# Kernel optimization log

Measured on AMD Instinct MI355X. Metric: run time of the kernel, lower is better.

Reference implementation:

```python
import jax, jax.numpy as jnp
import numpy as np


def setup_inputs() -> dict:
    key = jax.random.key(0)
    k_x, k_f1, k_f2, k_b = jax.random.split(key, 4)
    N, D = 2097152, 64  # batch rows, in_features = out_features = 8*8
    x = jax.random.normal(k_x, (N, D), dtype=jnp.float32)
    factor1 = jax.random.normal(k_f1, (8, 8), dtype=jnp.float32)
    factor2 = jax.random.normal(k_f2, (8, 8), dtype=jnp.float32)
    bias = jax.random.normal(k_b, (D,), dtype=jnp.float32)
    return {"x": x, "factor1": factor1, "factor2": factor2, "bias": bias}


def reference(x, factor1, factor2, bias):
    # weight = kron(ones((1,1)), factor1, factor2) == kron(factor1, factor2)
    # shape: [8*8, 8*8] = [64, 64]
    w = jnp.kron(factor1, factor2)
    # F.linear(x, w, bias) = x @ w.T + bias
    return x @ w.T + bias
```

## Files before the change

### kernel.cpp

```cpp
#include <hip/hip_runtime.h>


__global__ __launch_bounds__(256) void kron_linear_kernel(
    const float* __restrict__ x,
    const float* __restrict__ f1,
    const float* __restrict__ f2,
    const float* __restrict__ bias,
    float* __restrict__ out,
    int n_rows)
{
    int row = blockIdx.x * 256 + threadIdx.x;
    if (row >= n_rows) return;

    const float* xr = x + (size_t)row * 64;
    float* orow = out + (size_t)row * 64;

    float T[8][8];
#pragma unroll
    for (int i1 = 0; i1 < 8; ++i1) {
        float4 a = *(const float4*)(xr + i1 * 8);
        float4 b = *(const float4*)(xr + i1 * 8 + 4);
        float xv[8] = {a.x, a.y, a.z, a.w, b.x, b.y, b.z, b.w};
#pragma unroll
        for (int j2 = 0; j2 < 8; ++j2) {
            float acc = 0.f;
#pragma unroll
            for (int i2 = 0; i2 < 8; ++i2)
                acc += xv[i2] * f2[j2 * 8 + i2];
            T[i1][j2] = acc;
        }
    }

#pragma unroll
    for (int j1 = 0; j1 < 8; ++j1) {
        float o[8];
#pragma unroll
        for (int j2 = 0; j2 < 8; ++j2) o[j2] = bias[j1 * 8 + j2];
#pragma unroll
        for (int i1 = 0; i1 < 8; ++i1) {
            float w = f1[j1 * 8 + i1];
#pragma unroll
            for (int j2 = 0; j2 < 8; ++j2)
                o[j2] += w * T[i1][j2];
        }
        float4 s0 = {o[0], o[1], o[2], o[3]};
        float4 s1 = {o[4], o[5], o[6], o[7]};
        *(float4*)(orow + j1 * 8)     = s0;
        *(float4*)(orow + j1 * 8 + 4) = s1;
    }
}

extern "C" void kernel_launch(void* const* d_in, const int* in_sizes, int n_in,
                              void* d_out, int out_size, void* d_ws, size_t ws_size,
                              hipStream_t stream) {
    const float* x    = (const float*)d_in[0];
    const float* f1   = (const float*)d_in[1];
    const float* f2   = (const float*)d_in[2];
    const float* bias = (const float*)d_in[3];
    float* out = (float*)d_out;

    int n_rows = out_size / 64;
    int blocks = (n_rows + 255) / 256;
    kron_linear_kernel<<<blocks, 256, 0, stream>>>(x, f1, f2, bias, out, n_rows);
}
```

Baseline: 996.5 us.

## Stage row tiles through swizzled LDS for coalesced loads and stores

Each block now handles 128 rows. It copies the input tile into LDS with direct global-to-LDS 16-byte loads using an XOR swizzle, so global reads are fully coalesced. The computation is split across two threads per row, each producing half of the output columns. Results are written back to LDS and then stored to global memory coalesced. This adds barriers and 32KB of LDS per block, which may limit occupancy, and keeps a fallback path for the partial tail tile.

```diff
diff --git a/kernel.cpp b/kernel.cpp
--- a/kernel.cpp
+++ b/kernel.cpp
@@ -1,7 +1,12 @@
 #include <hip/hip_runtime.h>
 
 
-__global__ __launch_bounds__(256) void kron_linear_kernel(
+#define GLD_TO_LDS16(gptr, lptr)                                          \
+    __builtin_amdgcn_global_load_lds(                                     \
+        (const __attribute__((address_space(1))) unsigned int*)(gptr),    \
+        (__attribute__((address_space(3))) unsigned int*)(lptr), 16, 0, 0)
+
+__global__ __launch_bounds__(256, 4) void kron_linear_kernel(
     const float* __restrict__ x,
     const float* __restrict__ f1,
     const float* __restrict__ f2,
@@ -9,44 +14,109 @@
     float* __restrict__ out,
     int n_rows)
 {
-    int row = blockIdx.x * 256 + threadIdx.x;
-    if (row >= n_rows) return;
+    const int t = threadIdx.x;
+    const long long tile_row0 = (long long)blockIdx.x * 128;
 
-    const float* xr = x + (size_t)row * 64;
-    float* orow = out + (size_t)row * 64;
+    __shared__ float4 lds[2048];
 
-    float T[8][8];
+    if (tile_row0 + 128 <= (long long)n_rows) {
+        const int r = t & 127;
+        const int h = t >> 7;
+
+        const float4* xg = (const float4*)x + tile_row0 * 16;
 #pragma unroll
-    for (int i1 = 0; i1 < 8; ++i1) {
-        float4 a = *(const float4*)(xr + i1 * 8);
-        float4 b = *(const float4*)(xr + i1 * 8 + 4);
-        float xv[8] = {a.x, a.y, a.z, a.w, b.x, b.y, b.z, b.w};
+        for (int k = 0; k < 8; ++k) {
+            int s  = k * 256 + t;
+            int sr = s >> 4;
+            int c  = (s & 15) ^ (sr & 15);
+            GLD_TO_LDS16(xg + (sr * 16 + c), &lds[s]);
+        }
+        __syncthreads();
+
+        const float* f2h = f2 + (h * 4) * 8;
+        float T[8][4];
+        const int rbase = r * 16;
+        const int rs = r & 15;
 #pragma unroll
-        for (int j2 = 0; j2 < 8; ++j2) {
-            float acc = 0.f;
+        for (int i1 = 0; i1 < 8; ++i1) {
+            float4 a = lds[rbase + ((2 * i1)     ^ rs)];
+            float4 b = lds[rbase + ((2 * i1 + 1) ^ rs)];
+            float xv[8] = {a.x, a.y, a.z, a.w, b.x, b.y, b.z, b.w};
 #pragma unroll
-            for (int i2 = 0; i2 < 8; ++i2)
-                acc += xv[i2] * f2[j2 * 8 + i2];
-            T[i1][j2] = acc;
+            for (int jj = 0; jj < 4; ++jj) {
+                float acc = 0.f;
+#pragma unroll
+                for (int i2 = 0; i2 < 8; ++i2)
+                    acc += xv[i2] * f2h[jj * 8 + i2];
+                T[i1][jj] = acc;
+            }
         }
-    }
+        __syncthreads();
 
 #pragma unroll
-    for (int j1 = 0; j1 < 8; ++j1) {
-        float o[8];
+        for (int j1 = 0; j1 < 8; ++j1) {
+            float o0 = bias[j1 * 8 + 4 * h + 0];
+            float o1 = bias[j1 * 8 + 4 * h + 1];
+            float o2 = bias[j1 * 8 + 4 * h + 2];
+            float o3 = bias[j1 * 8 + 4 * h + 3];
 #pragma unroll
-        for (int j2 = 0; j2 < 8; ++j2) o[j2] = bias[j1 * 8 + j2];
+            for (int i1 = 0; i1 < 8; ++i1) {
+                float w = f1[j1 * 8 + i1];
+                o0 += w * T[i1][0];
+                o1 += w * T[i1][1];
+                o2 += w * T[i1][2];
+                o3 += w * T[i1][3];
+            }
+            int c = 2 * j1 + h;
+            lds[rbase + (c ^ rs)] = make_float4(o0, o1, o2, o3);
+        }
+        __syncthreads();
+
+        float4* og = (float4*)out + tile_row0 * 16;
+#pragma unroll
+        for (int k = 0; k < 8; ++k) {
+            int s  = k * 256 + t;
+            int sr = s >> 4;
+            int c  = (s & 15) ^ (sr & 15);
+            og[sr * 16 + c] = lds[s];
+        }
+    } else {
+        long long row = tile_row0 + t;
+        if (row >= (long long)n_rows) return;
+
+        const float* xr = x + (size_t)row * 64;
+        float* orow = out + (size_t)row * 64;
+
+        float T[8][8];
 #pragma unroll
         for (int i1 = 0; i1 < 8; ++i1) {
-            float w = f1[j1 * 8 + i1];
+            float4 a = *(const float4*)(xr + i1 * 8);
+            float4 b = *(const float4*)(xr + i1 * 8 + 4);
+            float xv[8] = {a.x, a.y, a.z, a.w, b.x, b.y, b.z, b.w};
 #pragma unroll
-            for (int j2 = 0; j2 < 8; ++j2)
-                o[j2] += w * T[i1][j2];
+            for (int j2 = 0; j2 < 8; ++j2) {
+                float acc = 0.f;
+#pragma unroll
+                for (int i2 = 0; i2 < 8; ++i2)
+                    acc += xv[i2] * f2[j2 * 8 + i2];
+                T[i1][j2] = acc;
+            }
         }
-        float4 s0 = {o[0], o[1], o[2], o[3]};
-        float4 s1 = {o[4], o[5], o[6], o[7]};
-        *(float4*)(orow + j1 * 8)     = s0;
-        *(float4*)(orow + j1 * 8 + 4) = s1;
+#pragma unroll
+        for (int j1 = 0; j1 < 8; ++j1) {
+            float o[8];
+#pragma unroll
+            for (int j2 = 0; j2 < 8; ++j2) o[j2] = bias[j1 * 8 + j2];
+#pragma unroll
+            for (int i1 = 0; i1 < 8; ++i1) {
+                float w = f1[j1 * 8 + i1];
+#pragma unroll
+                for (int j2 = 0; j2 < 8; ++j2)
+                    o[j2] += w * T[i1][j2];
+            }
+            *(float4*)(orow + j1 * 8)     = make_float4(o[0], o[1], o[2], o[3]);
+            *(float4*)(orow + j1 * 8 + 4) = make_float4(o[4], o[5], o[6], o[7]);
+        }
     }
 }
 
@@ -60,6 +130,6 @@
     float* out = (float*)d_out;
 
     int n_rows = out_size / 64;
-    int blocks = (n_rows + 255) / 256;
+    int blocks = (n_rows + 127) / 128;
     kron_linear_kernel<<<blocks, 256, 0, stream>>>(x, f1, f2, bias, out, n_rows);
 }
```

New measurement: 855.2 us. 14.2% less time.
